# Performance work log

Hardware: AMD Instinct MI355X
Metric: run time of the kernel (lower is better)

## Reference

```python
import jax, jax.numpy as jnp
import numpy as np

I, H, NH, A = 128, 2048, 2, 4   # input_size, hidden_size, n_hidden, alpha_dim
K = 2 * A * A                   # per-position theta entries
B = 8192


def make_masks():
    # MADE sequential-ordering masks, identical to DART.create_masks
    inp = np.arange(I)
    degrees = [inp] + [np.arange(H) % (I - 1) for _ in range(NH + 1)] + [np.arange(I) - 1]
    masks = [(d1[:, None] >= d0[None, :]).astype(np.float32)
             for d0, d1 in zip(degrees[:-1], degrees[1:])]
    # last mask repeated per theta entry: repeat(1, K).view(-1, H) == row-repeat
    masks[-1] = np.repeat(masks[-1], K, axis=0)
    return [jnp.asarray(m) for m in masks]


def setup_inputs() -> dict:
    key = jax.random.key(0)
    ks = jax.random.split(key, 5)
    x = jax.random.normal(ks[0], (B, I), dtype=jnp.float32)

    def lin(k, out_dim, in_dim):
        kw, kb = jax.random.split(k)
        s = 1.0 / np.sqrt(in_dim)
        W = jax.random.uniform(kw, (out_dim, in_dim), minval=-s, maxval=s, dtype=jnp.float32)
        b = jax.random.uniform(kb, (out_dim,), minval=-s, maxval=s, dtype=jnp.float32)
        return W, b

    W0, b0 = lin(ks[1], H, I)
    W1, b1 = lin(ks[2], H, H)
    W2, b2 = lin(ks[3], H, H)
    W3, b3 = lin(ks[4], I * K, H)
    return dict(x=x, W0=W0, b0=b0, W1=W1, b1=b1, W2=W2, b2=b2, W3=W3, b3=b3)


def logexpmm(a, b):
    # log-domain matmul: out[..., i, j] = logsumexp_k(a[..., i, k] + b[..., k, j])
    return jax.nn.logsumexp(a[..., :, :, None] + b[..., None, :, :], axis=-2)


def reference(x, W0, b0, W1, b1, W2, b2, W3, b3):
    m = make_masks()
    h = jax.nn.relu(x @ (m[0] * W0).T + b0)
    h = jax.nn.relu(h @ (m[1] * W1).T + b1)
    h = jax.nn.relu(h @ (m[2] * W2).T + b2)
    theta = (h @ (m[3] * W3).T + b3).reshape(-1, I, 2, A, A)
    mu, alpha = theta[:, :, 0], theta[:, :, 1]  # (B, I, A, A)

    LOG2PI = float(np.log(2.0 * np.pi))
    xe = x[:, :, None, None]
    # Normal(mu, exp(alpha)).log_prob(x) - log(alpha_dim)
    logp = (-0.5 * ((xe - mu) * jnp.exp(-alpha)) ** 2
            - alpha - 0.5 * LOG2PI - jnp.log(jnp.float32(A)))

    first = logp[:, 0, 0:1]        # (B, 1, A)
    last = logp[:, -1, :, 0:1]     # (B, A, 1)
    inner = jnp.swapaxes(logp[:, 1:-1], 0, 1)  # (I-2, B, A, A)

    def step(carry, mtx):
        return logexpmm(carry, mtx), None

    prod, _ = jax.lax.scan(step, inner[0], inner[1:])
    return logexpmm(first, logexpmm(prod, last))  # (B, 1, 1)
```

## Files before the change

### kernel.cpp

```cpp
#include <hip/hip_runtime.h>
#include <hip/hip_bf16.h>
#include <cstdint>
#include <cstddef>

#define AS1 __attribute__((address_space(1)))
#define AS3 __attribute__((address_space(3)))

typedef __bf16 bf16x8  __attribute__((ext_vector_type(8)));
typedef float  floatx4 __attribute__((ext_vector_type(4)));

__device__ __forceinline__ void load_lds16(const void* g, void* l) {
    __builtin_amdgcn_global_load_lds((AS1 void*)g, (AS3 void*)l, 16, 0, 0);
}

__device__ __forceinline__ float fexp2(float x) { return __builtin_amdgcn_exp2f(x); }
__device__ __forceinline__ float flog2(float x) { return __builtin_amdgcn_logf(x); }

#define LOG2E 1.4426950408889634f
#define LN2   0.6931471805599453f
#define C0K   2.3052328943245633f

__device__ __forceinline__ float logp2(float xv, float mu, float al) {
    float e = fexp2(-al * LOG2E);
    float z = (xv - mu) * e;
    return (-0.5f * z * z - al - C0K) * LOG2E;
}
__device__ __forceinline__ float lse4(float a0, float a1, float a2, float a3) {
    float mx = fmaxf(fmaxf(a0, a1), fmaxf(a2, a3));
    return mx + flog2(fexp2(a0 - mx) + fexp2(a1 - mx) +
                      fexp2(a2 - mx) + fexp2(a3 - mx));
}
__device__ __forceinline__ void lmm4(const float* Aa, const float* Bb, float* D) {
#pragma unroll
    for (int r = 0; r < 4; ++r)
#pragma unroll
        for (int c = 0; c < 4; ++c)
            D[r * 4 + c] = lse4(Aa[r * 4 + 0] + Bb[0 * 4 + c],
                                Aa[r * 4 + 1] + Bb[1 * 4 + c],
                                Aa[r * 4 + 2] + Bb[2 * 4 + c],
                                Aa[r * 4 + 3] + Bb[3 * 4 + c]);
}

__device__ __forceinline__ int resp_s(int p) {
    return p < 272 ? p / 17 : 16 + ((p - 272) >> 4);
}
__device__ __forceinline__ int invp_s(int p) {
    if (p < 272) { int d = p / 17; int r = p - d * 17;
                   return r < 16 ? d + r * 127 : 2032 + d; }
    int d = 16 + ((p - 272) >> 4); int j = (p - 272) & 15;
    return d + j * 127;
}
__device__ __forceinline__ int cnt_le(int D) {
    return D < 16 ? (D + 1) * 17 : 272 + ((D - 15) << 4);
}

__global__ __launch_bounds__(256)
void prep_all(const float* __restrict__ x,  const float* __restrict__ W0,
              const float* __restrict__ W1, const float* __restrict__ W2,
              const float* __restrict__ W3,
              __bf16* __restrict__ xb,  __bf16* __restrict__ w0m,
              __bf16* __restrict__ w1m, __bf16* __restrict__ w2m,
              __bf16* __restrict__ w3m)
{
    __shared__ float lds[2048];
    const int blk = blockIdx.x;
    const int tid = threadIdx.x;
    const int t8  = tid * 8;

    if (blk < 640) {
        bf16x8 o;
        if (blk < 512) {
            size_t base = (size_t)blk * 2048 + t8;
            floatx4 a = *(const floatx4*)(x + base);
            floatx4 b = *(const floatx4*)(x + base + 4);
#pragma unroll
            for (int j = 0; j < 4; ++j) { o[j] = (__bf16)a[j]; o[4 + j] = (__bf16)b[j]; }
            *(bf16x8*)(xb + base) = o;
        } else {
            long idx = (long)(blk - 512) * 2048 + t8;
            int p_n = (int)(idx >> 7);
            int c   = (int)(idx & 127);
            int dg  = resp_s(p_n);
            const float* s = W0 + (long)invp_s(p_n) * 128 + c;
            floatx4 a = *(const floatx4*)s;
            floatx4 b = *(const floatx4*)(s + 4);
#pragma unroll
            for (int j = 0; j < 8; ++j) {
                float v = j < 4 ? a[j] : b[j - 4];
                o[j] = (__bf16)((dg >= c + j) ? v : 0.0f);
            }
            *(bf16x8*)(w0m + idx) = o;
        }
        return;
    }

    const float* srow; __bf16* drow; int deg_n; bool strict;
    if (blk < 2688) {
        int p_n = blk - 640;
        srow = W1 + (size_t)invp_s(p_n) * 2048; drow = w1m + (size_t)p_n * 2048;
        deg_n = resp_s(p_n); strict = false;
    } else if (blk < 4736) {
        int p_n = blk - 2688;
        srow = W2 + (size_t)invp_s(p_n) * 2048; drow = w2m + (size_t)p_n * 2048;
        deg_n = resp_s(p_n); strict = false;
    } else {
        int n = blk - 4736;
        srow = W3 + (size_t)n * 2048; drow = w3m + (size_t)n * 2048;
        deg_n = n >> 5; strict = true;
    }
    floatx4 a = *(const floatx4*)(srow + t8);
    floatx4 b = *(const floatx4*)(srow + t8 + 4);
    *(floatx4*)&lds[t8]     = a;
    *(floatx4*)&lds[t8 + 4] = b;
    __syncthreads();
    bf16x8 o;
#pragma unroll
    for (int j = 0; j < 8; ++j) {
        int p = t8 + j;
        float v = lds[invp_s(p)];
        int dg = resp_s(p);
        bool keep = strict ? (deg_n > dg) : (deg_n >= dg);
        o[j] = (__bf16)(keep ? v : 0.0f);
    }
    *(bf16x8*)(drow + t8) = o;
}

template <bool RELU, bool OBF16, bool TLAYOUT, bool PERMBIAS, int LMODE>
__global__ __launch_bounds__(256, 4)
void gemm_bt(const __bf16* __restrict__ A, const __bf16* __restrict__ Bw,
             const float* __restrict__ bias, void* __restrict__ Cout,
             int N, int K)
{
    __shared__ __align__(16) __bf16 lsA[128 * 64];
    __shared__ __align__(16) __bf16 lsB[128 * 64];
    const int tid  = threadIdx.x;
    const int wave = tid >> 6;
    const int lane = tid & 63;
    const int bm = blockIdx.x;
    const int bn = (gridDim.y - 1) - blockIdx.y;
    const int wm = wave >> 1, wn = wave & 1;

    const int r8 = lane >> 3;
    const int cb = (lane & 7) ^ r8;
    const __bf16* gsrc[8];
    __bf16* ldst[8];
#pragma unroll
    for (int t = 0; t < 8; ++t) {
        int j = wave * 8 + t;
        if (j < 16) {
            int row = bm * 128 + j * 8 + r8;
            gsrc[t] = A + (size_t)row * K + cb * 8;
            ldst[t] = lsA + j * 512;
        } else {
            int jj = j - 16;
            int row = bn * 128 + jj * 8 + r8;
            gsrc[t] = Bw + (size_t)row * K + cb * 8;
            ldst[t] = lsB + jj * 512;
        }
    }

    const int fr  = lane & 15;
    const int ks  = lane >> 4;
    const int sx  = fr & 7;
    const int sl0 = ((ks)     ^ sx) * 8;
    const int sl1 = ((4 + ks) ^ sx) * 8;
    const __bf16* arow[4];
    const __bf16* brow[4];
#pragma unroll
    for (int i = 0; i < 4; ++i) {
        arow[i] = lsA + (wm * 64 + i * 16 + fr) * 64;
        brow[i] = lsB + (wn * 64 + i * 16 + fr) * 64;
    }

    floatx4 acc[4][4];
    const floatx4 vzero = {0.f, 0.f, 0.f, 0.f};
#pragma unroll
    for (int mi = 0; mi < 4; ++mi)
#pragma unroll
        for (int ni = 0; ni < 4; ++ni) acc[mi][ni] = vzero;

    const int nk = K >> 6;
    int limit;
    if (LMODE == 0)      limit = (cnt_le(resp_s(bn * 128 + 127)) + 63) >> 6;
    else if (LMODE == 1) { int D = 4 * bn + 2; if (D > 126) D = 126;
                           limit = (cnt_le(D) + 63) >> 6; }
    else                 limit = (resp_s(bn * 128 + 127) + 64) >> 6;
    if (limit > nk) limit = nk;

    for (int it = 0; it < limit; ++it) {
        const int kt = it << 6;
        __syncthreads();
#pragma unroll
        for (int t = 0; t < 8; ++t)
            load_lds16((const void*)(gsrc[t] + kt), (void*)ldst[t]);
        __syncthreads();
        bf16x8 af[4], bf[4];
#pragma unroll
        for (int i = 0; i < 4; ++i) af[i] = *(const bf16x8*)(arow[i] + sl0);
#pragma unroll
        for (int i = 0; i < 4; ++i) bf[i] = *(const bf16x8*)(brow[i] + sl0);
#pragma unroll
        for (int mi = 0; mi < 4; ++mi)
#pragma unroll
            for (int ni = 0; ni < 4; ++ni)
                acc[mi][ni] = __builtin_amdgcn_mfma_f32_16x16x32_bf16(
                    af[mi], bf[ni], acc[mi][ni], 0, 0, 0);
#pragma unroll
        for (int i = 0; i < 4; ++i) af[i] = *(const bf16x8*)(arow[i] + sl1);
#pragma unroll
        for (int i = 0; i < 4; ++i) bf[i] = *(const bf16x8*)(brow[i] + sl1);
#pragma unroll
        for (int mi = 0; mi < 4; ++mi)
#pragma unroll
            for (int ni = 0; ni < 4; ++ni)
                acc[mi][ni] = __builtin_amdgcn_mfma_f32_16x16x32_bf16(
                    af[mi], bf[ni], acc[mi][ni], 0, 0, 0);
    }

    const int cn  = lane & 15;
    const int cr4 = (lane >> 4) * 4;
#pragma unroll
    for (int ni = 0; ni < 4; ++ni) {
        int col = bn * 128 + wn * 64 + ni * 16 + cn;
        float bv = bias[PERMBIAS ? invp_s(col) : col];
#pragma unroll
        for (int mi = 0; mi < 4; ++mi) {
            int row0 = bm * 128 + wm * 64 + mi * 16 + cr4;
#pragma unroll
            for (int q = 0; q < 4; ++q) {
                float v = acc[mi][ni][q] + bv;
                if (RELU) v = fmaxf(v, 0.f);
                if (TLAYOUT) {
                    size_t addr = (size_t)(bm * 2 + wm) * ((size_t)N * 64)
                                + (size_t)(col >> 5) * 2048
                                + (size_t)(mi * 16 + cr4 + q) * 32 + (col & 31);
                    ((__bf16*)Cout)[addr] = (__bf16)v;
                } else if (OBF16) {
                    ((__bf16*)Cout)[(size_t)(row0 + q) * N + col] = (__bf16)v;
                } else {
                    ((float*)Cout)[(size_t)(row0 + q) * N + col] = v;
                }
            }
        }
    }
}

#define CFENCE() asm volatile("" ::: "memory")
#define BARX()  do { CFENCE(); __builtin_amdgcn_s_barrier(); CFENCE(); } while (0)
#define WVM2()  asm volatile("s_waitcnt vmcnt(2)" ::: "memory")
#define WVM0()  asm volatile("s_waitcnt vmcnt(0)" ::: "memory")
#define WLGK()  asm volatile("s_waitcnt lgkmcnt(0)" ::: "memory")

template <bool RELU, bool OBF16, bool TLAYOUT, bool PERMBIAS, int LMODE>
__global__ __launch_bounds__(512)
void gemm8p(const __bf16* __restrict__ A, const __bf16* __restrict__ Bw,
            const float* __restrict__ bias, void* __restrict__ Cout,
            int N, int K)
{
    __shared__ __align__(16) __bf16 ls[2 * 24576];
    const int tid  = threadIdx.x;
    const int wave = tid >> 6;
    const int lane = tid & 63;
    const int bm = blockIdx.x;
    const int bn = (gridDim.y - 1) - blockIdx.y;
    const int wm = wave >> 1, wn = wave & 1;

    const int l8 = lane >> 3;
    const int cb = (lane & 7) ^ l8;
    const __bf16* gA[2][2];  int dA[2][2];
    const __bf16* gB[2];     int dB[2];
#pragma unroll
    for (int h = 0; h < 2; ++h)
#pragma unroll
        for (int s = 0; s < 2; ++s) {
            int rt = h * 128 + wave * 16 + s * 8;
            gA[h][s] = A + (size_t)(bm * 256 + rt + l8) * K + cb * 8;
            dA[h][s] = rt * 64;
        }
#pragma unroll
    for (int s = 0; s < 2; ++s) {
        int rt = wave * 16 + s * 8;
        gB[s] = Bw + (size_t)(bn * 128 + rt + l8) * K + cb * 8;
        dB[s] = 16384 + rt * 64;
    }

#define STG_A(buf, kt) do { \
    load_lds16((const void*)(gA[0][0] + (kt)), (void*)(ls + (buf)*24576 + dA[0][0])); \
    load_lds16((const void*)(gA[0][1] + (kt)), (void*)(ls + (buf)*24576 + dA[0][1])); \
    load_lds16((const void*)(gA[1][0] + (kt)), (void*)(ls + (buf)*24576 + dA[1][0])); \
    load_lds16((const void*)(gA[1][1] + (kt)), (void*)(ls + (buf)*24576 + dA[1][1])); } while (0)
#define STG_B(buf, kt) do { \
    load_lds16((const void*)(gB[0] + (kt)), (void*)(ls + (buf)*24576 + dB[0])); \
    load_lds16((const void*)(gB[1] + (kt)), (void*)(ls + (buf)*24576 + dB[1])); } while (0)

    const int fr  = lane & 15;
    const int ks  = lane >> 4;
    const int sx  = fr & 7;
    const int sl0 = ((ks)     ^ sx) * 8;
    const int sl1 = ((4 + ks) ^ sx) * 8;
    int aoff[4], boff[4];
#pragma unroll
    for (int i = 0; i < 4; ++i) {
        aoff[i] = (wm * 64 + i * 16 + fr) * 64;
        boff[i] = 16384 + (wn * 64 + i * 16 + fr) * 64;
    }

    floatx4 acc[4][4];
    const floatx4 vzero = {0.f, 0.f, 0.f, 0.f};
#pragma unroll
    for (int mi = 0; mi < 4; ++mi)
#pragma unroll
        for (int ni = 0; ni < 4; ++ni) acc[mi][ni] = vzero;

    bf16x8 bfr[4][2], afr[2][2];

#define DSRD_B(buf) do { \
    _Pragma("unroll") \
    for (int ni = 0; ni < 4; ++ni) { \
        bfr[ni][0] = *(const bf16x8*)(ls + (buf)*24576 + boff[ni] + sl0); \
        bfr[ni][1] = *(const bf16x8*)(ls + (buf)*24576 + boff[ni] + sl1); } } while (0)
#define DSRD_A(buf, q) do { \
    _Pragma("unroll") \
    for (int j = 0; j < 2; ++j) { \
        afr[j][0] = *(const bf16x8*)(ls + (buf)*24576 + aoff[2*(q)+j] + sl0); \
        afr[j][1] = *(const bf16x8*)(ls + (buf)*24576 + aoff[2*(q)+j] + sl1); } } while (0)
#define MFMA16(q) do { \
    __builtin_amdgcn_s_setprio(1); \
    _Pragma("unroll") \
    for (int j = 0; j < 2; ++j) \
    _Pragma("unroll") \
    for (int ni = 0; ni < 4; ++ni) { \
        acc[2*(q)+j][ni] = __builtin_amdgcn_mfma_f32_16x16x32_bf16( \
            afr[j][0], bfr[ni][0], acc[2*(q)+j][ni], 0, 0, 0); \
        acc[2*(q)+j][ni] = __builtin_amdgcn_mfma_f32_16x16x32_bf16( \
            afr[j][1], bfr[ni][1], acc[2*(q)+j][ni], 0, 0, 0); } \
    __builtin_amdgcn_s_setprio(0); } while (0)

    const int nk = K >> 6;
    int limit;
    if (LMODE == 0)      limit = (cnt_le(resp_s(bn * 128 + 127)) + 63) >> 6;
    else if (LMODE == 1) { int D = 4 * bn + 2; if (D > 126) D = 126;
                           limit = (cnt_le(D) + 63) >> 6; }
    else                 limit = (resp_s(bn * 128 + 127) + 64) >> 6;
    if (limit > nk) limit = nk;
    const int NT = limit;

    STG_B(0, 0);
    STG_A(0, 0);
    if (NT > 1) { STG_B(1, 64); WVM2(); } else { WVM0(); }
    BARX();

    for (int t = 0; ; t += 2) {
        const int kt1 = (t + 1) << 6, kt2 = (t + 2) << 6, kt3 = (t + 3) << 6;
        const bool has1 = t + 1 < NT, has2 = t + 2 < NT, has3 = t + 3 < NT;

        DSRD_B(0);
        DSRD_A(0, 0);
        if (has1) STG_A(1, kt1);
        BARX(); WLGK();
        MFMA16(0);
        BARX();

        DSRD_A(0, 1);
        if (has2) STG_B(0, kt2);
        BARX(); WLGK();
        MFMA16(1);
        if (!has1) break;
        if (has2) WVM2(); else WVM0();
        BARX();

        DSRD_B(1);
        DSRD_A(1, 0);
        if (has2) STG_A(0, kt2);
        BARX(); WLGK();
        MFMA16(0);
        BARX();

        DSRD_A(1, 1);
        if (has3) STG_B(1, kt3);
        BARX(); WLGK();
        MFMA16(1);
        if (!has2) break;
        if (has3) WVM2(); else WVM0();
        BARX();
    }

    const int cn  = lane & 15;
    const int cr4 = (lane >> 4) * 4;
#pragma unroll
    for (int ni = 0; ni < 4; ++ni) {
        int col = bn * 128 + wn * 64 + ni * 16 + cn;
        float bv = bias[PERMBIAS ? invp_s(col) : col];
#pragma unroll
        for (int mi = 0; mi < 4; ++mi) {
            int row0 = bm * 256 + wm * 64 + mi * 16 + cr4;
#pragma unroll
            for (int q = 0; q < 4; ++q) {
                float v = acc[mi][ni][q] + bv;
                if (RELU) v = fmaxf(v, 0.f);
                if (TLAYOUT) {
                    size_t addr = (size_t)(bm * 4 + wm) * ((size_t)N * 64)
                                + (size_t)(col >> 5) * 2048
                                + (size_t)(mi * 16 + cr4 + q) * 32 + (col & 31);
                    ((__bf16*)Cout)[addr] = (__bf16)v;
                } else if (OBF16) {
                    ((__bf16*)Cout)[(size_t)(row0 + q) * N + col] = (__bf16)v;
                } else {
                    ((float*)Cout)[(size_t)(row0 + q) * N + col] = v;
                }
            }
        }
    }
#undef STG_A
#undef STG_B
#undef DSRD_B
#undef DSRD_A
#undef MFMA16
}

__global__ __launch_bounds__(448)
void chain_all(const __bf16* __restrict__ th2,
               const float* __restrict__ x,
               float* __restrict__ out)
{
    __shared__ float xs[32 * 129];
    __shared__ float Pl[32 * 238];
    const int tid = threadIdx.x;
    const int blk = blockIdx.x;

    for (int idx = tid; idx < 4096; idx += 448) {
        int bl = idx >> 7, i = idx & 127;
        xs[bl * 129 + i] = x[(size_t)blk * 4096 + idx];
    }
    __syncthreads();

    const int s  = tid >> 5;
    const int bl = tid & 31;
    const int b64 = (blk & 1) * 32 + bl;
    const __bf16* tb = th2 + (size_t)(blk >> 1) * 262144 + (size_t)b64 * 32;

    {
        const int i0 = 1 + s * 9;
        const __bf16* tp = tb + (size_t)i0 * 2048;
        float M[4][4];
#pragma unroll
        for (int r = 0; r < 4; ++r)
#pragma unroll
            for (int c = 0; c < 4; ++c) M[r][c] = (r == c) ? 0.f : -1e30f;

        for (int ii = 0; ii < 9; ++ii) {
            bf16x8 v0 = *(const bf16x8*)(tp);
            bf16x8 v1 = *(const bf16x8*)(tp + 8);
            bf16x8 v2 = *(const bf16x8*)(tp + 16);
            bf16x8 v3 = *(const bf16x8*)(tp + 24);
            float mu[16], al[16];
#pragma unroll
            for (int j = 0; j < 8; ++j) {
                mu[j] = (float)v0[j]; mu[8 + j] = (float)v1[j];
                al[j] = (float)v2[j]; al[8 + j] = (float)v3[j];
            }
            float xv = xs[bl * 129 + i0 + ii];
            tp += 2048;
            float lp[16];
#pragma unroll
            for (int j = 0; j < 16; ++j) lp[j] = logp2(xv, mu[j], al[j]);
            float Mn[4][4];
#pragma unroll
            for (int r = 0; r < 4; ++r)
#pragma unroll
                for (int c = 0; c < 4; ++c)
                    Mn[r][c] = lse4(M[r][0] + lp[0 + c], M[r][1] + lp[4 + c],
                                    M[r][2] + lp[8 + c], M[r][3] + lp[12 + c]);
#pragma unroll
            for (int r = 0; r < 4; ++r)
#pragma unroll
                for (int c = 0; c < 4; ++c) M[r][c] = Mn[r][c];
        }
        float* pb = Pl + bl * 238 + s * 17;
#pragma unroll
        for (int r = 0; r < 4; ++r)
#pragma unroll
            for (int c = 0; c < 4; ++c) pb[r * 4 + c] = M[r][c];
    }
    __syncthreads();

    float Q[16];
    if (tid < 224) {
        const float* base = Pl + bl * 238;
        lmm4(base + (2 * s) * 17, base + (2 * s + 1) * 17, Q);
    }
    __syncthreads();
    if (tid < 224) {
        float* dst = Pl + bl * 238 + s * 17;
#pragma unroll
        for (int e = 0; e < 16; ++e) dst[e] = Q[e];
    }
    __syncthreads();

    if (tid < 32) {
        const float* base = Pl + tid * 238;
        float M[16], T[16];
#pragma unroll
        for (int e = 0; e < 16; ++e) M[e] = base[e];
#pragma unroll
        for (int j = 1; j < 7; ++j) {
            lmm4(M, base + j * 17, T);
#pragma unroll
            for (int e = 0; e < 16; ++e) M[e] = T[e];
        }
        const int bb64 = (blk & 1) * 32 + tid;
        const __bf16* tbb = th2 + (size_t)(blk >> 1) * 262144 + (size_t)bb64 * 32;
        float x0 = xs[tid * 129 + 0];
        float xl = xs[tid * 129 + 127];
        float last[4], t4[4], f4[4];
#pragma unroll
        for (int c = 0; c < 4; ++c)
            last[c] = logp2(xl, (float)tbb[(size_t)127 * 2048 + c * 4],
                                (float)tbb[(size_t)127 * 2048 + 16 + c * 4]);
#pragma unroll
        for (int r = 0; r < 4; ++r)
            t4[r] = lse4(M[r * 4 + 0] + last[0], M[r * 4 + 1] + last[1],
                         M[r * 4 + 2] + last[2], M[r * 4 + 3] + last[3]);
#pragma unroll
        for (int r = 0; r < 4; ++r)
            f4[r] = logp2(x0, (float)tbb[r], (float)tbb[16 + r]);
        out[blk * 32 + tid] = LN2 * lse4(f4[0] + t4[0], f4[1] + t4[1],
                                         f4[2] + t4[2], f4[3] + t4[3]);
    }
}

extern "C" void kernel_launch(void* const* d_in, const int* in_sizes, int n_in,
                              void* d_out, int out_size, void* d_ws, size_t ws_size,
                              hipStream_t stream)
{
    (void)in_sizes; (void)n_in; (void)out_size; (void)ws_size;
    const float* x  = (const float*)d_in[0];
    const float* W0 = (const float*)d_in[1];
    const float* b0 = (const float*)d_in[2];
    const float* W1 = (const float*)d_in[3];
    const float* b1 = (const float*)d_in[4];
    const float* W2 = (const float*)d_in[5];
    const float* b2 = (const float*)d_in[6];
    const float* W3 = (const float*)d_in[7];
    const float* b3 = (const float*)d_in[8];

    char* ws = (char*)d_ws;
    const size_t MB = 1024 * 1024;
    __bf16* h2  = (__bf16*)(ws + 0);
    __bf16* xb  = (__bf16*)(ws + 32 * MB);
    __bf16* w0m = (__bf16*)(ws + 34 * MB);
    __bf16* w1m = (__bf16*)(ws + 35 * MB);
    __bf16* w2m = (__bf16*)(ws + 43 * MB);
    __bf16* th  = (__bf16*)(ws + 0);
    __bf16* w3m = (__bf16*)(ws + 64 * MB);
    __bf16* h1  = (__bf16*)(ws + 80 * MB);
    __bf16* h3  = h1;

    prep_all<<<8832, 256, 0, stream>>>(x, W0, W1, W2, W3, xb, w0m, w1m, w2m, w3m);

    gemm_bt<true, true, false, true, 2><<<dim3(64, 16), 256, 0, stream>>>(
        xb, w0m, b0, h1, 2048, 128);
    gemm8p<true, true, false, true, 0><<<dim3(32, 16), 512, 0, stream>>>(
        h1, w1m, b1, h2, 2048, 2048);
    gemm8p<true, true, false, true, 0><<<dim3(32, 16), 512, 0, stream>>>(
        h2, w2m, b2, h3, 2048, 2048);
    gemm_bt<false, false, true, false, 1><<<dim3(64, 32), 256, 0, stream>>>(
        h3, w3m, b3, th, 4096, 2048);

    chain_all<<<256, 448, 0, stream>>>(th, x, (float*)d_out);
}
```

Baseline: 314.6 us.

## Add LDS-free K=128 first-layer GEMM and widen chain kernel to 18 segments

```diff
diff --git a/kernel.cpp b/kernel.cpp
--- a/kernel.cpp
+++ b/kernel.cpp
@@ -123,6 +123,82 @@
         o[j] = (__bf16)(keep ? v : 0.0f);
     }
     *(bf16x8*)(drow + t8) = o;
+}
+
+template <bool PERMBIAS>
+__global__ __launch_bounds__(256, 8)
+void gemm_k128(const __bf16* __restrict__ A, const __bf16* __restrict__ Bw,
+               const float* __restrict__ bias, __bf16* __restrict__ Cout,
+               int N)
+{
+    const int K = 128;
+    const int tid  = threadIdx.x;
+    const int wave = tid >> 6;
+    const int lane = tid & 63;
+    const int bm = blockIdx.x;
+    const int bn = (gridDim.y - 1) - blockIdx.y;
+    const int wm = wave >> 1, wn = wave & 1;
+    const int fr = lane & 15, ks = lane >> 4;
+
+    const __bf16* arow[4];
+    const __bf16* brow[4];
+#pragma unroll
+    for (int i = 0; i < 4; ++i) {
+        arow[i] = A  + (size_t)(bm * 128 + wm * 64 + i * 16 + fr) * K + ks * 8;
+        brow[i] = Bw + (size_t)(bn * 128 + wn * 64 + i * 16 + fr) * K + ks * 8;
+    }
+
+    floatx4 acc[4][4];
+    const floatx4 vzero = {0.f, 0.f, 0.f, 0.f};
+#pragma unroll
+    for (int mi = 0; mi < 4; ++mi)
+#pragma unroll
+        for (int ni = 0; ni < 4; ++ni) acc[mi][ni] = vzero;
+
+    int limit = (resp_s(bn * 128 + 127) + 64) >> 6;
+    if (limit > 2) limit = 2;
+
+    for (int it = 0; it < limit; ++it) {
+        const int kt = it << 6;
+        bf16x8 af[4], bf[4];
+#pragma unroll
+        for (int i = 0; i < 4; ++i) af[i] = *(const bf16x8*)(arow[i] + kt);
+#pragma unroll
+        for (int i = 0; i < 4; ++i) bf[i] = *(const bf16x8*)(brow[i] + kt);
+#pragma unroll
+        for (int mi = 0; mi < 4; ++mi)
+#pragma unroll
+            for (int ni = 0; ni < 4; ++ni)
+                acc[mi][ni] = __builtin_amdgcn_mfma_f32_16x16x32_bf16(
+                    af[mi], bf[ni], acc[mi][ni], 0, 0, 0);
+#pragma unroll
+        for (int i = 0; i < 4; ++i) af[i] = *(const bf16x8*)(arow[i] + kt + 32);
+#pragma unroll
+        for (int i = 0; i < 4; ++i) bf[i] = *(const bf16x8*)(brow[i] + kt + 32);
+#pragma unroll
+        for (int mi = 0; mi < 4; ++mi)
+#pragma unroll
+            for (int ni = 0; ni < 4; ++ni)
+                acc[mi][ni] = __builtin_amdgcn_mfma_f32_16x16x32_bf16(
+                    af[mi], bf[ni], acc[mi][ni], 0, 0, 0);
+    }
+
+    const int cn  = lane & 15;
+    const int cr4 = (lane >> 4) * 4;
+#pragma unroll
+    for (int ni = 0; ni < 4; ++ni) {
+        int col = bn * 128 + wn * 64 + ni * 16 + cn;
+        float bv = bias[PERMBIAS ? invp_s(col) : col];
+#pragma unroll
+        for (int mi = 0; mi < 4; ++mi) {
+            int row0 = bm * 128 + wm * 64 + mi * 16 + cr4;
+#pragma unroll
+            for (int q = 0; q < 4; ++q) {
+                float v = fmaxf(acc[mi][ni][q] + bv, 0.f);
+                Cout[(size_t)(row0 + q) * N + col] = (__bf16)v;
+            }
+        }
+    }
 }
 
 template <bool RELU, bool OBF16, bool TLAYOUT, bool PERMBIAS, int LMODE>
@@ -418,17 +494,17 @@
 #undef MFMA16
 }
 
-__global__ __launch_bounds__(448)
+__global__ __launch_bounds__(576)
 void chain_all(const __bf16* __restrict__ th2,
                const float* __restrict__ x,
                float* __restrict__ out)
 {
     __shared__ float xs[32 * 129];
-    __shared__ float Pl[32 * 238];
+    __shared__ float Pl[32 * 306];
     const int tid = threadIdx.x;
     const int blk = blockIdx.x;
 
-    for (int idx = tid; idx < 4096; idx += 448) {
+    for (int idx = tid; idx < 4096; idx += 576) {
         int bl = idx >> 7, i = idx & 127;
         xs[bl * 129 + i] = x[(size_t)blk * 4096 + idx];
     }
@@ -440,7 +516,7 @@
     const __bf16* tb = th2 + (size_t)(blk >> 1) * 262144 + (size_t)b64 * 32;
 
     {
-        const int i0 = 1 + s * 9;
+        const int i0 = 1 + s * 7;
         const __bf16* tp = tb + (size_t)i0 * 2048;
         float M[4][4];
 #pragma unroll
@@ -448,7 +524,7 @@
 #pragma unroll
             for (int c = 0; c < 4; ++c) M[r][c] = (r == c) ? 0.f : -1e30f;
 
-        for (int ii = 0; ii < 9; ++ii) {
+        for (int ii = 0; ii < 7; ++ii) {
             bf16x8 v0 = *(const bf16x8*)(tp);
             bf16x8 v1 = *(const bf16x8*)(tp + 8);
             bf16x8 v2 = *(const bf16x8*)(tp + 16);
@@ -476,7 +552,7 @@
 #pragma unroll
                 for (int c = 0; c < 4; ++c) M[r][c] = Mn[r][c];
         }
-        float* pb = Pl + bl * 238 + s * 17;
+        float* pb = Pl + bl * 306 + s * 17;
 #pragma unroll
         for (int r = 0; r < 4; ++r)
 #pragma unroll
@@ -485,25 +561,25 @@
     __syncthreads();
 
     float Q[16];
-    if (tid < 224) {
-        const float* base = Pl + bl * 238;
+    if (tid < 288) {
+        const float* base = Pl + bl * 306;
         lmm4(base + (2 * s) * 17, base + (2 * s + 1) * 17, Q);
     }
     __syncthreads();
-    if (tid < 224) {
-        float* dst = Pl + bl * 238 + s * 17;
+    if (tid < 288) {
+        float* dst = Pl + bl * 306 + s * 17;
 #pragma unroll
         for (int e = 0; e < 16; ++e) dst[e] = Q[e];
     }
     __syncthreads();
 
     if (tid < 32) {
-        const float* base = Pl + tid * 238;
+        const float* base = Pl + tid * 306;
         float M[16], T[16];
 #pragma unroll
         for (int e = 0; e < 16; ++e) M[e] = base[e];
 #pragma unroll
-        for (int j = 1; j < 7; ++j) {
+        for (int j = 1; j < 9; ++j) {
             lmm4(M, base + j * 17, T);
 #pragma unroll
             for (int e = 0; e < 16; ++e) M[e] = T[e];
@@ -558,8 +634,7 @@
 
     prep_all<<<8832, 256, 0, stream>>>(x, W0, W1, W2, W3, xb, w0m, w1m, w2m, w3m);
 
-    gemm_bt<true, true, false, true, 2><<<dim3(64, 16), 256, 0, stream>>>(
-        xb, w0m, b0, h1, 2048, 128);
+    gemm_k128<true><<<dim3(64, 16), 256, 0, stream>>>(xb, w0m, b0, h1, 2048);
     gemm8p<true, true, false, true, 0><<<dim3(32, 16), 512, 0, stream>>>(
         h1, w1m, b1, h2, 2048, 2048);
     gemm8p<true, true, false, true, 0><<<dim3(32, 16), 512, 0, stream>>>(
@@ -567,5 +642,5 @@
     gemm_bt<false, false, true, false, 1><<<dim3(64, 32), 256, 0, stream>>>(
         h3, w3m, b3, th, 4096, 2048);
 
-    chain_all<<<256, 448, 0, stream>>>(th, x, (float*)d_out);
-}
+    chain_all<<<256, 576, 0, stream>>>(th, x, (float*)d_out);
+}
```

Result: slower. 403.7 us (+28.3%).
